# Performance work log

Measured on AMD Instinct MI355X. Metric: run time of the kernel, lower is better.

Reference implementation:

```python
import jax, jax.numpy as jnp
import numpy as np

B, T, D = 8, 2048, 512


def setup_inputs() -> dict:
    key = jax.random.key(0)
    k1, _ = jax.random.split(key)
    h = jax.random.normal(k1, (B, T, D), dtype=jnp.float32)
    k = jnp.ones((), dtype=jnp.float32)  # scalar learned decay param, init='ones'
    return {"h": h, "k": k}


def reference(h, k):
    # h: [B, T, D], k: scalar
    Tn = h.shape[1]
    h_cum = jnp.cumsum(h, axis=1)                                   # [B,T,D]
    h_prev = jnp.pad(h[:, :-1, :], ((0, 0), (1, 0), (0, 0)))        # shift right by 1
    delta = h_cum - h_prev
    delta_mag = jnp.linalg.norm(delta, axis=-1)                      # [B,T]
    t = jnp.arange(Tn)[:, None]
    j = jnp.arange(Tn)[None, :]
    dist = jnp.abs(t - j).astype(jnp.float32)
    decay = jnp.exp(-jax.nn.softplus(k) * dist) * (j <= t)           # [T,T] causal decay
    # importance_{b,i,j} = delta_mag_{b,i} * decay_{i,j}; factor delta_mag out of einsum
    context = jnp.einsum('ij,bjd->bid', decay, h)                    # [B,T,D]
    return jnp.abs(delta_mag[..., None] * context)
```

## Files before the change

kernel.cpp:

```cpp
#include <hip/hip_runtime.h>
#include <math.h>

#define BB 8
#define TT 2048
#define DD 512
#define LL 16
#define CC (TT / LL)
#define D4 (DD / 4)
#define SCT 64
#define NSC (TT / SCT)
#define CPS (SCT / LL)

typedef float floatx4 __attribute__((ext_vector_type(4)));

__device__ __forceinline__ float get_s(const float* kp) {
    float k = *kp;
    return (k > 20.0f) ? k : log1pf(expf(k));
}

__global__ __launch_bounds__(D4) void kA_stats(
    const float* __restrict__ h, const float* __restrict__ kp,
    float* __restrict__ csum, float* __restrict__ cend,
    float* __restrict__ ssum, float* __restrict__ send)
{
    const int blk = blockIdx.x;
    const int b = blk / NSC, sc = blk % NSC;
    const int tid = threadIdx.x;
    const float s   = get_s(kp);
    const float a   = expf(-s);
    const float a16 = expf(-s * (float)LL);

    const float4* hp = reinterpret_cast<const float4*>(h)
                     + (size_t)(b * TT + sc * SCT) * D4 + tid;

    float Sx = 0.f, Sy = 0.f, Sz = 0.f, Sw = 0.f;
    float Ex = 0.f, Ey = 0.f, Ez = 0.f, Ew = 0.f;

    #pragma unroll
    for (int j = 0; j < CPS; j++) {
        float sx = 0.f, sy = 0.f, sz = 0.f, sw = 0.f;
        float ex = 0.f, ey = 0.f, ez = 0.f, ew = 0.f;
        #pragma unroll
        for (int i = 0; i < LL; i++) {
            float4 x = hp[(size_t)(j * LL + i) * D4];
            sx += x.x; sy += x.y; sz += x.z; sw += x.w;
            ex = fmaf(a, ex, x.x);
            ey = fmaf(a, ey, x.y);
            ez = fmaf(a, ez, x.z);
            ew = fmaf(a, ew, x.w);
        }
        const size_t wi = (size_t)(b * CC + sc * CPS + j) * D4 + tid;
        reinterpret_cast<float4*>(csum)[wi] = make_float4(sx, sy, sz, sw);
        reinterpret_cast<float4*>(cend)[wi] = make_float4(ex, ey, ez, ew);
        Sx += sx; Sy += sy; Sz += sz; Sw += sw;
        Ex = fmaf(a16, Ex, ex);
        Ey = fmaf(a16, Ey, ey);
        Ez = fmaf(a16, Ez, ez);
        Ew = fmaf(a16, Ew, ew);
    }
    const size_t wi = (size_t)(b * NSC + sc) * D4 + tid;
    reinterpret_cast<float4*>(ssum)[wi] = make_float4(Sx, Sy, Sz, Sw);
    reinterpret_cast<float4*>(send)[wi] = make_float4(Ex, Ey, Ez, Ew);
}

__global__ __launch_bounds__(D4) void kB_out(
    const float* __restrict__ h, const float* __restrict__ kp,
    const float* __restrict__ csum, const float* __restrict__ cend,
    const float* __restrict__ ssum, const float* __restrict__ send,
    float* __restrict__ out)
{
    const int blk = blockIdx.x;
    const int b = blk / CC, c = blk % CC;
    const int sc = c / CPS, j = c & (CPS - 1);
    const int tid = threadIdx.x;
    const int wave = tid >> 6, lane = tid & 63;
    const int w64 = wave << 6;
    const float s   = get_s(kp);
    const float a   = expf(-s);
    const float a16 = expf(-s * (float)LL);
    const float aSC = expf(-s * (float)SCT);

    const int t0 = c * LL;
    const float4* hp = reinterpret_cast<const float4*>(h)
                     + (size_t)(b * TT + t0) * D4 + tid;

    __shared__ float4 stash[LL][D4];
    __shared__ float part[2][LL];

    #pragma unroll
    for (int i = 0; i < LL; i++) {
        __builtin_amdgcn_global_load_lds(
            (const __attribute__((address_space(1))) void*)(hp + (size_t)i * D4),
            (__attribute__((address_space(3))) void*)(&stash[i][w64]),
            16, 0, 0);
    }

    float px = 0.f, py = 0.f, pz = 0.f, pw = 0.f;
    if (t0 > 0) {
        float4 pv = *(hp - (ptrdiff_t)D4);
        px = pv.x; py = pv.y; pz = pv.z; pw = pv.w;
    }

    float cox = 0.f, coy = 0.f, coz = 0.f, cow = 0.f;
    float ccx = 0.f, ccy = 0.f, ccz = 0.f, ccw = 0.f;
    {
        const float4* ss4 = reinterpret_cast<const float4*>(ssum)
                          + (size_t)(b * NSC) * D4 + tid;
        const float4* se4 = reinterpret_cast<const float4*>(send)
                          + (size_t)(b * NSC) * D4 + tid;
        float w = 1.f;
        for (int p = sc - 1; p >= 0; --p) {
            float4 sv = ss4[(size_t)p * D4];
            float4 ev = se4[(size_t)p * D4];
            cox += sv.x; coy += sv.y; coz += sv.z; cow += sv.w;
            ccx = fmaf(w, ev.x, ccx);
            ccy = fmaf(w, ev.y, ccy);
            ccz = fmaf(w, ev.z, ccz);
            ccw = fmaf(w, ev.w, ccw);
            w *= aSC;
        }
    }
    {
        const float4* cs4 = reinterpret_cast<const float4*>(csum)
                          + (size_t)(b * CC + sc * CPS) * D4 + tid;
        const float4* ce4 = reinterpret_cast<const float4*>(cend)
                          + (size_t)(b * CC + sc * CPS) * D4 + tid;
        float wj = 1.f;
        float cIx = 0.f, cIy = 0.f, cIz = 0.f, cIw = 0.f;
        for (int p = j - 1; p >= 0; --p) {
            float4 sv = cs4[(size_t)p * D4];
            float4 ev = ce4[(size_t)p * D4];
            cox += sv.x; coy += sv.y; coz += sv.z; cow += sv.w;
            cIx = fmaf(wj, ev.x, cIx);
            cIy = fmaf(wj, ev.y, cIy);
            cIz = fmaf(wj, ev.z, cIz);
            cIw = fmaf(wj, ev.w, cIw);
            wj *= a16;
        }
        ccx = fmaf(wj, ccx, cIx);
        ccy = fmaf(wj, ccy, cIy);
        ccz = fmaf(wj, ccz, cIz);
        ccw = fmaf(wj, ccw, cIw);
    }

    __syncthreads();

    float r[LL];
    #pragma unroll
    for (int i = 0; i < LL; i++) {
        float4 x = stash[i][tid];
        cox += x.x; coy += x.y; coz += x.z; cow += x.w;
        float dx = cox - px, dy = coy - py, dz = coz - pz, dw = cow - pw;
        r[i] = dx * dx + dy * dy + dz * dz + dw * dw;
        px = x.x; py = x.y; pz = x.z; pw = x.w;
    }

    #pragma unroll
    for (int m = 1; m < 64; m <<= 1) {
        #pragma unroll
        for (int i = 0; i < LL; i++) r[i] += __shfl_xor(r[i], m, 64);
    }
    if (lane == 0) {
        #pragma unroll
        for (int i = 0; i < LL; i++) part[wave][i] = r[i];
    }
    __syncthreads();

    float mag[LL];
    #pragma unroll
    for (int i = 0; i < LL; i++) mag[i] = sqrtf(part[0][i] + part[1][i]);

    floatx4* op = reinterpret_cast<floatx4*>(out)
                + (size_t)(b * TT + t0) * D4 + tid;
    #pragma unroll
    for (int i = 0; i < LL; i++) {
        float4 x = stash[i][tid];
        ccx = fmaf(a, ccx, x.x);
        ccy = fmaf(a, ccy, x.y);
        ccz = fmaf(a, ccz, x.z);
        ccw = fmaf(a, ccw, x.w);
        float m = mag[i];
        floatx4 o;
        o.x = fabsf(m * ccx); o.y = fabsf(m * ccy);
        o.z = fabsf(m * ccz); o.w = fabsf(m * ccw);
        __builtin_nontemporal_store(o, op + (size_t)i * D4);
    }
}

extern "C" void kernel_launch(void* const* d_in, const int* in_sizes, int n_in,
                              void* d_out, int out_size, void* d_ws, size_t ws_size,
                              hipStream_t stream) {
    const float* h  = (const float*)d_in[0];
    const float* kp = (const float*)d_in[1];
    float* out = (float*)d_out;

    const size_t NC = (size_t)BB * CC * DD;
    const size_t NSb = (size_t)BB * NSC * DD;
    float* csum = (float*)d_ws;
    float* cend = csum + NC;
    float* ssum = cend + NC;
    float* send = ssum + NSb;

    kA_stats<<<dim3(BB * NSC), dim3(D4), 0, stream>>>(h, kp, csum, cend, ssum, send);
    kB_out  <<<dim3(BB * CC),  dim3(D4), 0, stream>>>(h, kp, csum, cend, ssum, send, out);
}
```

Before: 96.50 us.

## Add super-chunk exclusive prefix scan kernel to replace per-block carry loops

Adds a small middle kernel that turns the per-super-chunk sums and decayed ends into exclusive prefix carries in place. The output kernel then reads a single precomputed carry instead of looping over all earlier super-chunks, which removes the work that grew quadratically across blocks. The cost is one extra kernel launch and a serial 32-step scan run by only 32 blocks.

Result: no change. 98.20 us (+1.8%).

```diff
diff --git a/kernel.cpp b/kernel.cpp
--- a/kernel.cpp
+++ b/kernel.cpp
@@ -63,6 +63,30 @@
     reinterpret_cast<float4*>(send)[wi] = make_float4(Ex, Ey, Ez, Ew);
 }
 
+__global__ __launch_bounds__(128) void k2_sscan(
+    float* __restrict__ ssum, float* __restrict__ send,
+    const float* __restrict__ kp)
+{
+    const int g = blockIdx.x * 128 + threadIdx.x;
+    const int b = g >> 9;
+    const int d = g & (DD - 1);
+    const float s   = get_s(kp);
+    const float aSC = expf(-s * (float)SCT);
+
+    const size_t base = (size_t)b * NSC * DD + d;
+    float co = 0.f, cc = 0.f;
+    #pragma unroll
+    for (int p = 0; p < NSC; p++) {
+        const size_t idx = base + (size_t)p * DD;
+        float sv = ssum[idx];
+        float ev = send[idx];
+        ssum[idx] = co;
+        send[idx] = cc;
+        co += sv;
+        cc = fmaf(aSC, cc, ev);
+    }
+}
+
 __global__ __launch_bounds__(D4) void kB_out(
     const float* __restrict__ h, const float* __restrict__ kp,
     const float* __restrict__ csum, const float* __restrict__ cend,
@@ -78,7 +102,6 @@
     const float s   = get_s(kp);
     const float a   = expf(-s);
     const float a16 = expf(-s * (float)LL);
-    const float aSC = expf(-s * (float)SCT);
 
     const int t0 = c * LL;
     const float4* hp = reinterpret_cast<const float4*>(h)
@@ -101,24 +124,14 @@
         px = pv.x; py = pv.y; pz = pv.z; pw = pv.w;
     }
 
-    float cox = 0.f, coy = 0.f, coz = 0.f, cow = 0.f;
-    float ccx = 0.f, ccy = 0.f, ccz = 0.f, ccw = 0.f;
+    float cox, coy, coz, cow;
+    float ccx, ccy, ccz, ccw;
     {
-        const float4* ss4 = reinterpret_cast<const float4*>(ssum)
-                          + (size_t)(b * NSC) * D4 + tid;
-        const float4* se4 = reinterpret_cast<const float4*>(send)
-                          + (size_t)(b * NSC) * D4 + tid;
-        float w = 1.f;
-        for (int p = sc - 1; p >= 0; --p) {
-            float4 sv = ss4[(size_t)p * D4];
-            float4 ev = se4[(size_t)p * D4];
-            cox += sv.x; coy += sv.y; coz += sv.z; cow += sv.w;
-            ccx = fmaf(w, ev.x, ccx);
-            ccy = fmaf(w, ev.y, ccy);
-            ccz = fmaf(w, ev.z, ccz);
-            ccw = fmaf(w, ev.w, ccw);
-            w *= aSC;
-        }
+        const size_t si = (size_t)(b * NSC + sc) * D4 + tid;
+        float4 sv = reinterpret_cast<const float4*>(ssum)[si];
+        float4 ev = reinterpret_cast<const float4*>(send)[si];
+        cox = sv.x; coy = sv.y; coz = sv.z; cow = sv.w;
+        ccx = ev.x; ccy = ev.y; ccz = ev.z; ccw = ev.w;
     }
     {
         const float4* cs4 = reinterpret_cast<const float4*>(csum)
@@ -202,5 +215,6 @@
     float* send = ssum + NSb;
 
     kA_stats<<<dim3(BB * NSC), dim3(D4), 0, stream>>>(h, kp, csum, cend, ssum, send);
+    k2_sscan<<<dim3(BB * DD / 128), dim3(128), 0, stream>>>(ssum, send, kp);
     kB_out  <<<dim3(BB * CC),  dim3(D4), 0, stream>>>(h, kp, csum, cend, ssum, send, out);
 }
```
